# Kernel tuning notes

Hardware: AMD Instinct MI355X
Metric: run time of the kernel (lower is better)

The kernel has to match this reference:

```python
import jax, jax.numpy as jnp
import numpy as np

E, H, M, IN, T = 4, 64, 64, 32, 32      # e_size, hidden_state, message, in_size, target
HL = (128, 256, 128)                     # NNet hidden layers (priba's NNet default)
N_LAYERS = 3


def setup_inputs() -> dict:
    key = jax.random.key(0)
    ks = iter(jax.random.split(key, 64))
    B, N = 16, 128

    def w(shape, scale=0.1):
        return jax.random.normal(next(ks), shape, dtype=jnp.float32) * scale

    inp = {
        "h_in": jax.random.normal(next(ks), (B, N, IN), dtype=jnp.float32),
        "am": jax.random.normal(next(ks), (B, N, N, E), dtype=jnp.float32),
        "g_size": jax.random.randint(next(ks), (B,), 0, N),
    }
    # EdgeNetwork NNet: E -> 128 -> 256 -> 128 -> M*H
    dims_e = (E,) + HL + (M * H,)
    for i in range(4):
        inp[f"We{i}"] = w((dims_e[i], dims_e[i + 1]))
        inp[f"be{i}"] = w((dims_e[i + 1],))
    # GRU (torch nn.GRU, one layer, one step): input M, hidden H
    inp["Wih"] = w((3 * H, M)); inp["Whh"] = w((3 * H, H))
    inp["bih"] = w((3 * H,)); inp["bhh"] = w((3 * H,))
    # Readout NNets: i on [h_T, h_0] (H+IN -> T), j on h_T (H -> T)
    dims_i = (H + IN,) + HL + (T,)
    dims_j = (H,) + HL + (T,)
    for i in range(4):
        inp[f"Wi{i}"] = w((dims_i[i], dims_i[i + 1])); inp[f"bi{i}"] = w((dims_i[i + 1],))
        inp[f"Wj{i}"] = w((dims_j[i], dims_j[i + 1])); inp[f"bj{i}"] = w((dims_j[i + 1],))
    return inp


def _mlp(x, Ws, bs):
    for Wk, bk in zip(Ws[:-1], bs[:-1]):
        x = jax.nn.relu(x @ Wk + bk)
    return x @ Ws[-1] + bs[-1]


def reference(h_in, am, g_size,
              We0, be0, We1, be1, We2, be2, We3, be3,
              Wih, Whh, bih, bhh,
              Wi0, bi0, Wi1, bi1, Wi2, bi2, Wi3, bi3,
              Wj0, bj0, Wj1, bj1, Wj2, bj2, Wj3, bj3):
    B, N, _ = h_in.shape
    h = jnp.pad(h_in, ((0, 0), (0, 0), (0, H - IN)))            # pad to hidden size
    mask = (jnp.arange(N)[None, :] < g_size[:, None]).astype(h.dtype)[:, :, None]  # [B,N,1]

    # Edge-network hidden features; final linear layer is fused into the
    # message contraction to avoid materializing per-edge [M,H] matrices.
    f = am                                                       # [B,N,N,E]
    for Wk, bk in ((We0, be0), (We1, be1), (We2, be2)):
        f = jax.nn.relu(f @ Wk + bk)                             # [B,N,N,128]
    W3 = We3.reshape(HL[-1], M, H)                               # [128,M,H]
    b3 = be3.reshape(M, H)

    for _ in range(N_LAYERS):                                    # weight-tied GGNN steps
        # m[b,v,o] = sum_w (A(e_bvw) @ h_bw)[o], A = reshape(f @ We3 + be3)
        t = jnp.einsum('bvwk,bwi->bvki', f, h)                   # [B,N,128,H]
        msg = jnp.einsum('bvki,koi->bvo', t, W3)
        msg = msg + jnp.einsum('oi,bi->bo', b3, h.sum(1))[:, None, :]
        # single-step torch GRU update
        gi = msg @ Wih.T + bih
        gh = h @ Whh.T + bhh
        r = jax.nn.sigmoid(gi[..., :H] + gh[..., :H])
        z = jax.nn.sigmoid(gi[..., H:2 * H] + gh[..., H:2 * H])
        n = jnp.tanh(gi[..., 2 * H:] + r * gh[..., 2 * H:])
        h = (1.0 - z) * n + z * h
        h = h * mask

    # GGNN readout: sum_v mask * sigmoid(i([h_T, h_0])) * j(h_T), then log_softmax
    gate = jax.nn.sigmoid(_mlp(jnp.concatenate([h, h_in], -1),
                               (Wi0, Wi1, Wi2, Wi3), (bi0, bi1, bi2, bi3)))
    val = _mlp(h, (Wj0, Wj1, Wj2, Wj3), (bj0, bj1, bj2, bj3))
    res = (mask * gate * val).sum(1)                             # [B,T]
    return jax.nn.log_softmax(res, axis=1)
```

## Files before the change

kernel.cpp:

```cpp
#include <hip/hip_runtime.h>
#include <math.h>

#define B   16
#define N   128
#define E   4
#define H   64
#define M   64
#define IN_ 32
#define T   32
#define K1  128
#define K2  256
#define K3  128

typedef _Float16 f16;
typedef f16  f16x8 __attribute__((ext_vector_type(8)));
typedef float f32x4 __attribute__((ext_vector_type(4)));

#define MFMA16(a, b, c) __builtin_amdgcn_mfma_f32_16x16x32_f16(a, b, c, 0, 0, 0)

#define OFF_W1T   0
#define OFF_W2T   32768
#define OFF_WE3H  65536
#define OFF_RI0   589824
#define OFF_RI1   602112
#define OFF_RI2   634880
#define OFF_RI3   667648
#define OFF_RJ0   671744
#define OFF_RJ1   679936
#define OFF_RJ2   712704
#define OFF_RJ3   745472
#define WPACK_SZ  749568

union SmemU {
    struct { float xl[64][4]; f16 y1[64][136]; f16 y2[64][264]; } e;
    struct { f16 Al[128][72]; f16 Bl[128][72]; f16 Ol[128][136]; } pg;
    struct { float prt[4][64]; float hsum[64]; float bias[64]; } bi;
};

__global__ __launch_bounds__(256) void prep_kernel(
    const float* __restrict__ h_in,
    const float* __restrict__ We1, const float* __restrict__ We2,
    const float* __restrict__ We3,
    const float* __restrict__ Wi0, const float* __restrict__ Wi1,
    const float* __restrict__ Wi2, const float* __restrict__ Wi3,
    const float* __restrict__ Wj0, const float* __restrict__ Wj1,
    const float* __restrict__ Wj2, const float* __restrict__ Wj3,
    float* __restrict__ h, f16* __restrict__ h16, f16* __restrict__ hin16,
    f16* __restrict__ wp) {
    int idx = blockIdx.x * 256 + threadIdx.x;
    if (idx < B * N * H) {
        int i  = idx & (H - 1);
        int bn = idx >> 6;
        float v = (i < IN_) ? h_in[bn * IN_ + i] : 0.f;
        h[idx] = v;
        h16[idx] = (f16)v;
        if (i < IN_) hin16[bn * IN_ + i] = (f16)v;
    }
    if (idx >= WPACK_SZ) return;
    if (idx < OFF_W2T) {
        int j = idx >> 7, k = idx & 127;
        wp[idx] = (f16)We1[k * 256 + j];
    } else if (idx < OFF_WE3H) {
        int t = idx - OFF_W2T;
        int j = t >> 8, k = t & 255;
        wp[idx] = (f16)We2[k * 128 + j];
    } else if (idx < OFF_RI0) {
        wp[idx] = (f16)We3[idx - OFF_WE3H];
    } else if (idx < OFF_RI1) {
        int t = idx - OFF_RI0;
        int n = t / 96, c = t % 96;
        wp[idx] = (f16)Wi0[c * 128 + n];
    } else if (idx < OFF_RI2) {
        int t = idx - OFF_RI1;
        int n = t >> 7, k = t & 127;
        wp[idx] = (f16)Wi1[k * 256 + n];
    } else if (idx < OFF_RI3) {
        int t = idx - OFF_RI2;
        int n = t >> 8, k = t & 255;
        wp[idx] = (f16)Wi2[k * 128 + n];
    } else if (idx < OFF_RJ0) {
        int t = idx - OFF_RI3;
        int n = t >> 7, k = t & 127;
        wp[idx] = (f16)Wi3[k * 32 + n];
    } else if (idx < OFF_RJ1) {
        int t = idx - OFF_RJ0;
        int n = t >> 6, c = t & 63;
        wp[idx] = (f16)Wj0[c * 128 + n];
    } else if (idx < OFF_RJ2) {
        int t = idx - OFF_RJ1;
        int n = t >> 7, k = t & 127;
        wp[idx] = (f16)Wj1[k * 256 + n];
    } else if (idx < OFF_RJ3) {
        int t = idx - OFF_RJ2;
        int n = t >> 8, k = t & 255;
        wp[idx] = (f16)Wj2[k * 128 + n];
    } else {
        int t = idx - OFF_RJ3;
        int n = t >> 7, k = t & 127;
        wp[idx] = (f16)Wj3[k * 32 + n];
    }
}


__device__ void edge_body(SmemU& su, int tid, int tile,
                          const float* __restrict__ am,
                          const float* __restrict__ We0,
                          const float* __restrict__ be0,
                          const f16* __restrict__ W1t,
                          const float* __restrict__ be1,
                          const f16* __restrict__ W2t,
                          const float* __restrict__ be2,
                          f16* __restrict__ f) {
    int lane = tid & 63, wv = tid >> 6;
    long long g0 = (long long)tile * 64;

    ((float*)su.e.xl)[tid] = am[g0 * 4 + tid];
    __syncthreads();

    {
        int j = tid & 127, e0 = (tid >> 7) * 32;
        float w0 = We0[j], w1 = We0[128 + j], w2 = We0[256 + j], w3 = We0[384 + j];
        float bb = be0[j];
        #pragma unroll 8
        for (int e = e0; e < e0 + 32; ++e) {
            float v = bb + su.e.xl[e][0] * w0 + su.e.xl[e][1] * w1
                         + su.e.xl[e][2] * w2 + su.e.xl[e][3] * w3;
            su.e.y1[e][j] = (f16)fmaxf(v, 0.f);
        }
    }
    __syncthreads();

    int m = lane & 15, q = lane >> 4;

    {
        f32x4 acc[4][4];
        #pragma unroll
        for (int ct = 0; ct < 4; ++ct)
            #pragma unroll
            for (int rt = 0; rt < 4; ++rt) acc[ct][rt] = (f32x4){0.f, 0.f, 0.f, 0.f};
        #pragma unroll
        for (int s = 0; s < 4; ++s) {
            int k0 = s * 32 + q * 8;
            f16x8 afr[4], bfr[4];
            #pragma unroll
            for (int rt = 0; rt < 4; ++rt)
                afr[rt] = *(const f16x8*)&su.e.y1[rt * 16 + m][k0];
            #pragma unroll
            for (int ct = 0; ct < 4; ++ct) {
                int n = (wv * 4 + ct) * 16 + m;
                bfr[ct] = *(const f16x8*)(W1t + n * 128 + k0);
            }
            #pragma unroll
            for (int ct = 0; ct < 4; ++ct)
                #pragma unroll
                for (int rt = 0; rt < 4; ++rt)
                    acc[ct][rt] = MFMA16(afr[rt], bfr[ct], acc[ct][rt]);
        }
        #pragma unroll
        for (int ct = 0; ct < 4; ++ct) {
            int n = (wv * 4 + ct) * 16 + m;
            float bb = be1[n];
            #pragma unroll
            for (int rt = 0; rt < 4; ++rt)
                #pragma unroll
                for (int r = 0; r < 4; ++r) {
                    int row = rt * 16 + q * 4 + r;
                    su.e.y2[row][n] = (f16)fmaxf(acc[ct][rt][r] + bb, 0.f);
                }
        }
    }
    __syncthreads();

    {
        f32x4 acc[2][4];
        #pragma unroll
        for (int ct = 0; ct < 2; ++ct)
            #pragma unroll
            for (int rt = 0; rt < 4; ++rt) acc[ct][rt] = (f32x4){0.f, 0.f, 0.f, 0.f};
        #pragma unroll
        for (int s = 0; s < 8; ++s) {
            int k0 = s * 32 + q * 8;
            f16x8 afr[4], bfr[2];
            #pragma unroll
            for (int rt = 0; rt < 4; ++rt)
                afr[rt] = *(const f16x8*)&su.e.y2[rt * 16 + m][k0];
            #pragma unroll
            for (int ct = 0; ct < 2; ++ct) {
                int n = (wv * 2 + ct) * 16 + m;
                bfr[ct] = *(const f16x8*)(W2t + n * 256 + k0);
            }
            #pragma unroll
            for (int ct = 0; ct < 2; ++ct)
                #pragma unroll
                for (int rt = 0; rt < 4; ++rt)
                    acc[ct][rt] = MFMA16(afr[rt], bfr[ct], acc[ct][rt]);
        }
        #pragma unroll
        for (int ct = 0; ct < 2; ++ct) {
            int n = (wv * 2 + ct) * 16 + m;
            float bb = be2[n];
            #pragma unroll
            for (int rt = 0; rt < 4; ++rt)
                #pragma unroll
                for (int r = 0; r < 4; ++r) {
                    int row = rt * 16 + q * 4 + r;
                    su.e.y1[row][n] = (f16)fmaxf(acc[ct][rt][r] + bb, 0.f);
                }
        }
    }
    __syncthreads();

    #pragma unroll
    for (int j = 0; j < 4; ++j) {
        int c = tid + j * 256;
        int e = c >> 4, pp = c & 15;
        *(uint4*)(f + (g0 + e) * 128 + pp * 8) = *(const uint4*)&su.e.y1[e][pp * 8];
    }
}

__device__ void pgemm_body(SmemU& su, int tid, int ob, int nt,
                           const f16* __restrict__ h16,
                           const f16* __restrict__ We3h,
                           f16* __restrict__ P2) {
    int lane = tid & 63, wv = tid >> 6;

    #pragma unroll
    for (int j = 0; j < 4; ++j) {
        int c = tid + j * 256;
        int row = c >> 3, pp = c & 7;
        *(uint4*)&su.pg.Al[row][pp * 8] =
            *(const uint4*)(h16 + (size_t)(nt * 128 + row) * 64 + pp * 8);
    }
    #pragma unroll
    for (int j = 0; j < 4; ++j) {
        int c = tid + j * 256;
        int k = c >> 3, pp = c & 7;
        *(uint4*)&su.pg.Bl[k][pp * 8] =
            *(const uint4*)(We3h + ((size_t)(k * 64 + ob)) * 64 + pp * 8);
    }
    __syncthreads();

    int m = lane & 15, q = lane >> 4;
    f32x4 acc[2][8];
    #pragma unroll
    for (int ct = 0; ct < 2; ++ct)
        #pragma unroll
        for (int rt = 0; rt < 8; ++rt) acc[ct][rt] = (f32x4){0.f, 0.f, 0.f, 0.f};
    #pragma unroll
    for (int s = 0; s < 2; ++s) {
        int k0 = s * 32 + q * 8;
        f16x8 afr[8], bfr[2];
        #pragma unroll
        for (int rt = 0; rt < 8; ++rt)
            afr[rt] = *(const f16x8*)&su.pg.Al[rt * 16 + m][k0];
        #pragma unroll
        for (int ct = 0; ct < 2; ++ct)
            bfr[ct] = *(const f16x8*)&su.pg.Bl[(wv * 2 + ct) * 16 + m][k0];
        #pragma unroll
        for (int ct = 0; ct < 2; ++ct)
            #pragma unroll
            for (int rt = 0; rt < 8; ++rt)
                acc[ct][rt] = MFMA16(afr[rt], bfr[ct], acc[ct][rt]);
    }
    #pragma unroll
    for (int ct = 0; ct < 2; ++ct) {
        int col = (wv * 2 + ct) * 16 + m;
        #pragma unroll
        for (int rt = 0; rt < 8; ++rt)
            #pragma unroll
            for (int r = 0; r < 4; ++r)
                su.pg.Ol[rt * 16 + q * 4 + r][col] = (f16)acc[ct][rt][r];
    }
    __syncthreads();
    #pragma unroll
    for (int j = 0; j < 8; ++j) {
        int c = tid + j * 256;
        int row = c >> 4, pp = c & 15;
        *(uint4*)(P2 + ((size_t)(nt * 128 + row) * 64 + ob) * 128 + pp * 8) =
            *(const uint4*)&su.pg.Ol[row][pp * 8];
    }
}

__device__ void bias_body(SmemU& su, int tid, int b,
                          const float* __restrict__ h,
                          const float* __restrict__ be3,
                          float* __restrict__ biasb) {
    int i = tid & 63, wq = tid >> 6;
    float s = 0.f;
    for (int w = wq; w < N; w += 4) s += h[((size_t)(b * N + w)) * H + i];
    su.bi.prt[wq][i] = s;
    __syncthreads();
    if (tid < 64)
        su.bi.hsum[tid] = su.bi.prt[0][tid] + su.bi.prt[1][tid]
                        + su.bi.prt[2][tid] + su.bi.prt[3][tid];
    __syncthreads();
    if (tid < 64) {
        float sb = 0.f;
        #pragma unroll 4
        for (int ii = 0; ii < H; ++ii) sb += be3[tid * H + ii] * su.bi.hsum[ii];
        biasb[b * 64 + tid] = sb;
    }
}

__global__ __launch_bounds__(256, 2) void mega0_kernel(
    const float* __restrict__ am,
    const float* __restrict__ We0, const float* __restrict__ be0,
    const float* __restrict__ be1, const float* __restrict__ be2,
    const float* __restrict__ be3,
    const f16* __restrict__ wp,
    const float* __restrict__ h, const f16* __restrict__ h16,
    f16* __restrict__ f, f16* __restrict__ P2, float* __restrict__ biasb) {
    __shared__ SmemU su;
    int tid = threadIdx.x;
    int bid = blockIdx.x;
    if (bid < 4096) {
        edge_body(su, tid, bid, am, We0, be0, wp + OFF_W1T, be1, wp + OFF_W2T,
                  be2, f);
    } else if (bid < 5120) {
        int t = bid - 4096;
        pgemm_body(su, tid, t & 63, t >> 6, h16, wp + OFF_WE3H, P2);
    } else {
        bias_body(su, tid, bid - 5120, h, be3, biasb);
    }
}

__global__ __launch_bounds__(256, 2) void pg_bias_kernel(
    const float* __restrict__ be3, const f16* __restrict__ wp,
    const float* __restrict__ h, const f16* __restrict__ h16,
    f16* __restrict__ P2, float* __restrict__ biasb) {
    __shared__ SmemU su;
    int tid = threadIdx.x;
    int bid = blockIdx.x;
    if (bid < 1024) {
        pgemm_body(su, tid, bid & 63, bid >> 6, h16, wp + OFF_WE3H, P2);
    } else {
        bias_body(su, tid, bid - 1024, h, be3, biasb);
    }
}

__global__ __launch_bounds__(256, 2) void msg_mfma(
    const f16* __restrict__ f, const f16* __restrict__ P2,
    float* __restrict__ part) {
    __shared__ f16 Al[128][136];
    __shared__ f16 Bl[64][136];
    int tid = threadIdx.x, lane = tid & 63, wv = tid >> 6;
    int ws = blockIdx.x;
    int b  = blockIdx.y;
    int m = lane & 15, q = lane >> 4;

    f32x4 acc[2][4];
    #pragma unroll
    for (int rt = 0; rt < 2; ++rt)
        #pragma unroll
        for (int ct = 0; ct < 4; ++ct) acc[rt][ct] = (f32x4){0.f, 0.f, 0.f, 0.f};

    for (int wi = 0; wi < 4; ++wi) {
        int w = ws * 4 + wi;
        #pragma unroll
        for (int j = 0; j < 8; ++j) {
            int c = tid + j * 256;
            int v = c >> 4, pp = c & 15;
            *(uint4*)&Al[v][pp * 8] =
                *(const uint4*)(f + (((size_t)(b * 128 + v) * 128 + w) * 128) + pp * 8);
        }
        #pragma unroll
        for (int j = 0; j < 4; ++j) {
            int c = tid + j * 256;
            int o = c >> 4, pp = c & 15;
            *(uint4*)&Bl[o][pp * 8] =
                *(const uint4*)(P2 + (((size_t)(b * 128 + w) * 64 + o) * 128) + pp * 8);
        }
        __syncthreads();
        #pragma unroll
        for (int s = 0; s < 4; ++s) {
            int k0 = s * 32 + q * 8;
            f16x8 afr[2], bfr[4];
            #pragma unroll
            for (int rt = 0; rt < 2; ++rt)
                afr[rt] = *(const f16x8*)&Al[(wv * 2 + rt) * 16 + m][k0];
            #pragma unroll
            for (int ct = 0; ct < 4; ++ct)
                bfr[ct] = *(const f16x8*)&Bl[ct * 16 + m][k0];
            #pragma unroll
            for (int rt = 0; rt < 2; ++rt)
                #pragma unroll
                for (int ct = 0; ct < 4; ++ct)
                    acc[rt][ct] = MFMA16(afr[rt], bfr[ct], acc[rt][ct]);
        }
        __syncthreads();
    }
    float* pp = part + (size_t)ws * (2048 * 64);
    #pragma unroll
    for (int rt = 0; rt < 2; ++rt)
        #pragma unroll
        for (int ct = 0; ct < 4; ++ct) {
            int o = ct * 16 + m;
            #pragma unroll
            for (int r = 0; r < 4; ++r) {
                int v = (wv * 2 + rt) * 16 + q * 4 + r;
                pp[(size_t)(b * 128 + v) * 64 + o] = acc[rt][ct][r];
            }
        }
}

__global__ __launch_bounds__(192) void gru_kernel(
    const float* __restrict__ biasb, const float* __restrict__ part,
    float* __restrict__ h, f16* __restrict__ h16,
    const float* __restrict__ Wih, const float* __restrict__ Whh,
    const float* __restrict__ bih, const float* __restrict__ bhh,
    const int* __restrict__ g_size) {
    __shared__ float m_lds[M];
    __shared__ float h_lds[H];
    __shared__ float gi[3 * H], gh[3 * H];
    int tid = threadIdx.x;
    int bv  = blockIdx.x;
    int b = bv >> 7, v = bv & 127;

    if (tid < M) {
        float s = biasb[b * 64 + tid];
        #pragma unroll 8
        for (int sp = 0; sp < 32; ++sp)
            s += part[(size_t)sp * (2048 * 64) + bv * 64 + tid];
        m_lds[tid] = s;
    } else if (tid < M + H) {
        h_lds[tid - M] = h[bv * H + (tid - M)];
    }
    __syncthreads();

    {
        float si = bih[tid], sh = bhh[tid];
        const float* wi = Wih + tid * M;
        const float* wh = Whh + tid * H;
        #pragma unroll 4
        for (int k = 0; k < M; ++k) si += wi[k] * m_lds[k];
        #pragma unroll 4
        for (int k = 0; k < H; ++k) sh += wh[k] * h_lds[k];
        gi[tid] = si;
        gh[tid] = sh;
    }
    __syncthreads();
    if (tid < H) {
        float r = 1.f / (1.f + expf(-(gi[tid] + gh[tid])));
        float z = 1.f / (1.f + expf(-(gi[H + tid] + gh[H + tid])));
        float n = tanhf(gi[2 * H + tid] + r * gh[2 * H + tid]);
        float hv = (1.f - z) * n + z * h_lds[tid];
        float maskf = (v < g_size[b]) ? 1.f : 0.f;
        hv *= maskf;
        h[bv * H + tid] = hv;
        h16[bv * H + tid] = (f16)hv;
    }
}

__global__ __launch_bounds__(256, 4) void readout_mfma(
    const f16* __restrict__ h16, const f16* __restrict__ hin16,
    const int* __restrict__ g_size, const f16* __restrict__ wp,
    const float* __restrict__ bi0, const float* __restrict__ bi1,
    const float* __restrict__ bi2, const float* __restrict__ bi3,
    const float* __restrict__ bj0, const float* __restrict__ bj1,
    const float* __restrict__ bj2, const float* __restrict__ bj3,
    float* __restrict__ contrib) {
    __shared__ f16 Xl[32][104];
    __shared__ f16 A1[32][136];
    __shared__ f16 A2[32][264];
    __shared__ float Gl[32][36];
    const f16* Ri0 = wp + OFF_RI0; const f16* Ri1 = wp + OFF_RI1;
    const f16* Ri2 = wp + OFF_RI2; const f16* Ri3 = wp + OFF_RI3;
    const f16* Rj0 = wp + OFF_RJ0; const f16* Rj1 = wp + OFF_RJ1;
    const f16* Rj2 = wp + OFF_RJ2; const f16* Rj3 = wp + OFF_RJ3;
    int tid = threadIdx.x, lane = tid & 63, wv = tid >> 6;
    int m = lane & 15, q = lane >> 4;
    int r0 = blockIdx.x * 32;

    {
        int row = tid >> 3, pp = tid & 7;
        *(uint4*)&Xl[row][pp * 8] = *(const uint4*)(h16 + (size_t)(r0 + row) * 64 + pp * 8);
        if (tid < 128) {
            int row2 = tid >> 2, p2 = tid & 3;
            *(uint4*)&Xl[row2][64 + p2 * 8] =
                *(const uint4*)(hin16 + (size_t)(r0 + row2) * 32 + p2 * 8);
        }
    }
    __syncthreads();

    {
        f32x4 acc[2][2];
        #pragma unroll
        for (int ct = 0; ct < 2; ++ct)
            #pragma unroll
            for (int rt = 0; rt < 2; ++rt) acc[ct][rt] = (f32x4){0.f, 0.f, 0.f, 0.f};
        #pragma unroll
        for (int s = 0; s < 3; ++s) {
            int k0 = s * 32 + q * 8;
            f16x8 afr[2], bfr[2];
            #pragma unroll
            for (int rt = 0; rt < 2; ++rt) afr[rt] = *(const f16x8*)&Xl[rt * 16 + m][k0];
            #pragma unroll
            for (int ct = 0; ct < 2; ++ct)
                bfr[ct] = *(const f16x8*)(Ri0 + ((wv * 2 + ct) * 16 + m) * 96 + k0);
            #pragma unroll
            for (int ct = 0; ct < 2; ++ct)
                #pragma unroll
                for (int rt = 0; rt < 2; ++rt)
                    acc[ct][rt] = MFMA16(afr[rt], bfr[ct], acc[ct][rt]);
        }
        #pragma unroll
        for (int ct = 0; ct < 2; ++ct) {
            int n = (wv * 2 + ct) * 16 + m;
            float bb = bi0[n];
            #pragma unroll
            for (int rt = 0; rt < 2; ++rt)
                #pragma unroll
                for (int r = 0; r < 4; ++r)
                    A1[rt * 16 + q * 4 + r][n] = (f16)fmaxf(acc[ct][rt][r] + bb, 0.f);
        }
    }
    __syncthreads();

    {
        f32x4 acc[4][2];
        #pragma unroll
        for (int ct = 0; ct < 4; ++ct)
            #pragma unroll
            for (int rt = 0; rt < 2; ++rt) acc[ct][rt] = (f32x4){0.f, 0.f, 0.f, 0.f};
        #pragma unroll
        for (int s = 0; s < 4; ++s) {
            int k0 = s * 32 + q * 8;
            f16x8 afr[2], bfr[4];
            #pragma unroll
            for (int rt = 0; rt < 2; ++rt) afr[rt] = *(const f16x8*)&A1[rt * 16 + m][k0];
            #pragma unroll
            for (int ct = 0; ct < 4; ++ct)
                bfr[ct] = *(const f16x8*)(Ri1 + ((wv * 4 + ct) * 16 + m) * 128 + k0);
            #pragma unroll
            for (int ct = 0; ct < 4; ++ct)
                #pragma unroll
                for (int rt = 0; rt < 2; ++rt)
                    acc[ct][rt] = MFMA16(afr[rt], bfr[ct], acc[ct][rt]);
        }
        #pragma unroll
        for (int ct = 0; ct < 4; ++ct) {
            int n = (wv * 4 + ct) * 16 + m;
            float bb = bi1[n];
            #pragma unroll
            for (int rt = 0; rt < 2; ++rt)
                #pragma unroll
                for (int r = 0; r < 4; ++r)
                    A2[rt * 16 + q * 4 + r][n] = (f16)fmaxf(acc[ct][rt][r] + bb, 0.f);
        }
    }
    __syncthreads();

    {
        f32x4 acc[2][2];
        #pragma unroll
        for (int ct = 0; ct < 2; ++ct)
            #pragma unroll
            for (int rt = 0; rt < 2; ++rt) acc[ct][rt] = (f32x4){0.f, 0.f, 0.f, 0.f};
        #pragma unroll
        for (int s = 0; s < 8; ++s) {
            int k0 = s * 32 + q * 8;
            f16x8 afr[2], bfr[2];
            #pragma unroll
            for (int rt = 0; rt < 2; ++rt) afr[rt] = *(const f16x8*)&A2[rt * 16 + m][k0];
            #pragma unroll
            for (int ct = 0; ct < 2; ++ct)
                bfr[ct] = *(const f16x8*)(Ri2 + ((wv * 2 + ct) * 16 + m) * 256 + k0);
            #pragma unroll
            for (int ct = 0; ct < 2; ++ct)
                #pragma unroll
                for (int rt = 0; rt < 2; ++rt)
                    acc[ct][rt] = MFMA16(afr[rt], bfr[ct], acc[ct][rt]);
        }
        __syncthreads();
        #pragma unroll
        for (int ct = 0; ct < 2; ++ct) {
            int n = (wv * 2 + ct) * 16 + m;
            float bb = bi2[n];
            #pragma unroll
            for (int rt = 0; rt < 2; ++rt)
                #pragma unroll
                for (int r = 0; r < 4; ++r)
                    A1[rt * 16 + q * 4 + r][n] = (f16)fmaxf(acc[ct][rt][r] + bb, 0.f);
        }
    }
    __syncthreads();

    if (wv < 2) {
        f32x4 acc[2];
        acc[0] = (f32x4){0.f, 0.f, 0.f, 0.f};
        acc[1] = (f32x4){0.f, 0.f, 0.f, 0.f};
        int n = wv * 16 + m;
        #pragma unroll
        for (int s = 0; s < 4; ++s) {
            int k0 = s * 32 + q * 8;
            f16x8 bfr = *(const f16x8*)(Ri3 + n * 128 + k0);
            #pragma unroll
            for (int rt = 0; rt < 2; ++rt) {
                f16x8 afr = *(const f16x8*)&A1[rt * 16 + m][k0];
                acc[rt] = MFMA16(afr, bfr, acc[rt]);
            }
        }
        float bb = bi3[n];
        #pragma unroll
        for (int rt = 0; rt < 2; ++rt)
            #pragma unroll
            for (int r = 0; r < 4; ++r)
                Gl[rt * 16 + q * 4 + r][n] = 1.f / (1.f + expf(-(acc[rt][r] + bb)));
    }
    __syncthreads();

    {
        f32x4 acc[2][2];
        #pragma unroll
        for (int ct = 0; ct < 2; ++ct)
            #pragma unroll
            for (int rt = 0; rt < 2; ++rt) acc[ct][rt] = (f32x4){0.f, 0.f, 0.f, 0.f};
        #pragma unroll
        for (int s = 0; s < 2; ++s) {
            int k0 = s * 32 + q * 8;
            f16x8 afr[2], bfr[2];
            #pragma unroll
            for (int rt = 0; rt < 2; ++rt) afr[rt] = *(const f16x8*)&Xl[rt * 16 + m][k0];
            #pragma unroll
            for (int ct = 0; ct < 2; ++ct)
                bfr[ct] = *(const f16x8*)(Rj0 + ((wv * 2 + ct) * 16 + m) * 64 + k0);
            #pragma unroll
            for (int ct = 0; ct < 2; ++ct)
                #pragma unroll
                for (int rt = 0; rt < 2; ++rt)
                    acc[ct][rt] = MFMA16(afr[rt], bfr[ct], acc[ct][rt]);
        }
        __syncthreads();
        #pragma unroll
        for (int ct = 0; ct < 2; ++ct) {
            int n = (wv * 2 + ct) * 16 + m;
            float bb = bj0[n];
            #pragma unroll
            for (int rt = 0; rt < 2; ++rt)
                #pragma unroll
                for (int r = 0; r < 4; ++r)
                    A1[rt * 16 + q * 4 + r][n] = (f16)fmaxf(acc[ct][rt][r] + bb, 0.f);
        }
    }
    __syncthreads();

    {
        f32x4 acc[4][2];
        #pragma unroll
        for (int ct = 0; ct < 4; ++ct)
            #pragma unroll
            for (int rt = 0; rt < 2; ++rt) acc[ct][rt] = (f32x4){0.f, 0.f, 0.f, 0.f};
        #pragma unroll
        for (int s = 0; s < 4; ++s) {
            int k0 = s * 32 + q * 8;
            f16x8 afr[2], bfr[4];
            #pragma unroll
            for (int rt = 0; rt < 2; ++rt) afr[rt] = *(const f16x8*)&A1[rt * 16 + m][k0];
            #pragma unroll
            for (int ct = 0; ct < 4; ++ct)
                bfr[ct] = *(const f16x8*)(Rj1 + ((wv * 4 + ct) * 16 + m) * 128 + k0);
            #pragma unroll
            for (int ct = 0; ct < 4; ++ct)
                #pragma unroll
                for (int rt = 0; rt < 2; ++rt)
                    acc[ct][rt] = MFMA16(afr[rt], bfr[ct], acc[ct][rt]);
        }
        #pragma unroll
        for (int ct = 0; ct < 4; ++ct) {
            int n = (wv * 4 + ct) * 16 + m;
            float bb = bj1[n];
            #pragma unroll
            for (int rt = 0; rt < 2; ++rt)
                #pragma unroll
                for (int r = 0; r < 4; ++r)
                    A2[rt * 16 + q * 4 + r][n] = (f16)fmaxf(acc[ct][rt][r] + bb, 0.f);
        }
    }
    __syncthreads();

    {
        f32x4 acc[2][2];
        #pragma unroll
        for (int ct = 0; ct < 2; ++ct)
            #pragma unroll
            for (int rt = 0; rt < 2; ++rt) acc[ct][rt] = (f32x4){0.f, 0.f, 0.f, 0.f};
        #pragma unroll
        for (int s = 0; s < 8; ++s) {
            int k0 = s * 32 + q * 8;
            f16x8 afr[2], bfr[2];
            #pragma unroll
            for (int rt = 0; rt < 2; ++rt) afr[rt] = *(const f16x8*)&A2[rt * 16 + m][k0];
            #pragma unroll
            for (int ct = 0; ct < 2; ++ct)
                bfr[ct] = *(const f16x8*)(Rj2 + ((wv * 2 + ct) * 16 + m) * 256 + k0);
            #pragma unroll
            for (int ct = 0; ct < 2; ++ct)
                #pragma unroll
                for (int rt = 0; rt < 2; ++rt)
                    acc[ct][rt] = MFMA16(afr[rt], bfr[ct], acc[ct][rt]);
        }
        __syncthreads();
        #pragma unroll
        for (int ct = 0; ct < 2; ++ct) {
            int n = (wv * 2 + ct) * 16 + m;
            float bb = bj2[n];
            #pragma unroll
            for (int rt = 0; rt < 2; ++rt)
                #pragma unroll
                for (int r = 0; r < 4; ++r)
                    A1[rt * 16 + q * 4 + r][n] = (f16)fmaxf(acc[ct][rt][r] + bb, 0.f);
        }
    }
    __syncthreads();

    if (wv < 2) {
        f32x4 acc[2];
        acc[0] = (f32x4){0.f, 0.f, 0.f, 0.f};
        acc[1] = (f32x4){0.f, 0.f, 0.f, 0.f};
        int n = wv * 16 + m;
        #pragma unroll
        for (int s = 0; s < 4; ++s) {
            int k0 = s * 32 + q * 8;
            f16x8 bfr = *(const f16x8*)(Rj3 + n * 128 + k0);
            #pragma unroll
            for (int rt = 0; rt < 2; ++rt) {
                f16x8 afr = *(const f16x8*)&A1[rt * 16 + m][k0];
                acc[rt] = MFMA16(afr, bfr, acc[rt]);
            }
        }
        float bb = bj3[n];
        #pragma unroll
        for (int rt = 0; rt < 2; ++rt)
            #pragma unroll
            for (int r = 0; r < 4; ++r) {
                int row = rt * 16 + q * 4 + r;
                int rg = r0 + row;
                int b = rg >> 7, v = rg & 127;
                float maskf = (v < g_size[b]) ? 1.f : 0.f;
                contrib[(size_t)rg * T + n] = maskf * Gl[row][n] * (acc[rt][r] + bb);
            }
    }
}

__global__ __launch_bounds__(64) void finalize_kernel(const float* __restrict__ contrib,
                                                      float* __restrict__ out) {
    __shared__ float res[T];
    int b = blockIdx.x;
    int o = threadIdx.x;
    if (o < T) {
        float s = 0.f;
        for (int v = 0; v < N; ++v) s += contrib[(b * N + v) * T + o];
        res[o] = s;
    }
    __syncthreads();
    if (o < T) {
        float mx = res[0];
        for (int i = 1; i < T; ++i) mx = fmaxf(mx, res[i]);
        float se = 0.f;
        for (int i = 0; i < T; ++i) se += expf(res[i] - mx);
        out[b * T + o] = res[o] - mx - logf(se);
    }
}

extern "C" void kernel_launch(void* const* d_in, const int* in_sizes, int n_in,
                              void* d_out, int out_size, void* d_ws, size_t ws_size,
                              hipStream_t stream) {
    (void)in_sizes; (void)n_in; (void)out_size; (void)ws_size;
    const float* h_in = (const float*)d_in[0];
    const float* am   = (const float*)d_in[1];
    const int*   g_sz = (const int*)d_in[2];
    const float* We0 = (const float*)d_in[3],  *be0 = (const float*)d_in[4];
    const float* We1 = (const float*)d_in[5],  *be1 = (const float*)d_in[6];
    const float* We2 = (const float*)d_in[7],  *be2 = (const float*)d_in[8];
    const float* We3 = (const float*)d_in[9],  *be3 = (const float*)d_in[10];
    const float* Wih = (const float*)d_in[11], *Whh = (const float*)d_in[12];
    const float* bih = (const float*)d_in[13], *bhh = (const float*)d_in[14];
    const float* Wi0 = (const float*)d_in[15], *bi0 = (const float*)d_in[16];
    const float* Wj0 = (const float*)d_in[17], *bj0 = (const float*)d_in[18];
    const float* Wi1 = (const float*)d_in[19], *bi1 = (const float*)d_in[20];
    const float* Wj1 = (const float*)d_in[21], *bj1 = (const float*)d_in[22];
    const float* Wi2 = (const float*)d_in[23], *bi2 = (const float*)d_in[24];
    const float* Wj2 = (const float*)d_in[25], *bj2 = (const float*)d_in[26];
    const float* Wi3 = (const float*)d_in[27], *bi3 = (const float*)d_in[28];
    const float* Wj3 = (const float*)d_in[29], *bj3 = (const float*)d_in[30];

    float* out = (float*)d_out;

    f16*   f    = (f16*)d_ws;
    f16*   P2   = f + (size_t)33554432;
    float* part = (float*)(P2 + (size_t)16777216);
    float* h    = part + (size_t)4194304;
    float* biasb = h + 131072;
    float* contrib = biasb + 1024;
    f16*   h16  = (f16*)(contrib + 65536);
    f16*   hin16 = h16 + 131072;
    f16*   wp   = hin16 + 65536;

    prep_kernel<<<(WPACK_SZ + 255) / 256, 256, 0, stream>>>(
        h_in, We1, We2, We3, Wi0, Wi1, Wi2, Wi3, Wj0, Wj1, Wj2, Wj3,
        h, h16, hin16, wp);

    mega0_kernel<<<4096 + 1024 + 16, 256, 0, stream>>>(
        am, We0, be0, be1, be2, be3, wp, h, h16, f, P2, biasb);
    msg_mfma<<<dim3(32, 16), 256, 0, stream>>>(f, P2, part);
    gru_kernel<<<B * N, 192, 0, stream>>>(biasb, part, h, h16,
                                          Wih, Whh, bih, bhh, g_sz);

    for (int l = 1; l < 3; ++l) {
        pg_bias_kernel<<<1024 + 16, 256, 0, stream>>>(be3, wp, h, h16, P2, biasb);
        msg_mfma<<<dim3(32, 16), 256, 0, stream>>>(f, P2, part);
        gru_kernel<<<B * N, 192, 0, stream>>>(biasb, part, h, h16,
                                              Wih, Whh, bih, bhh, g_sz);
    }

    readout_mfma<<<64, 256, 0, stream>>>(h16, hin16, g_sz, wp,
                                         bi0, bi1, bi2, bi3,
                                         bj0, bj1, bj2, bj3, contrib);
    finalize_kernel<<<B, 64, 0, stream>>>(contrib, out);
}
```

Baseline: 412.1 us.

## Fuse message GEMM with GRU update and fold finalize into readout

Replaces the split-K message kernel plus separate GRU kernel with one kernel per (batch, 32-node tile). It accumulates messages over all neighbours in registers and then applies the GRU in place, which removes the fp32 partial-sum buffer and its reduction. The P-GEMM tile is halved to 64 rows to double its block count, and occupancy hints are raised. The log-softmax finalize moves into the last readout block via an atomic counter. The fused message kernel launches only 64 blocks that loop serially over 128 neighbours with two barriers each, so it risks leaving most of the GPU idle.

```diff
diff --git a/kernel.cpp b/kernel.cpp
--- a/kernel.cpp
+++ b/kernel.cpp
@@ -8,9 +8,6 @@
 #define M   64
 #define IN_ 32
 #define T   32
-#define K1  128
-#define K2  256
-#define K3  128
 
 typedef _Float16 f16;
 typedef f16  f16x8 __attribute__((ext_vector_type(8)));
@@ -33,8 +30,8 @@
 
 union SmemU {
     struct { float xl[64][4]; f16 y1[64][136]; f16 y2[64][264]; } e;
-    struct { f16 Al[128][72]; f16 Bl[128][72]; f16 Ol[128][136]; } pg;
-    struct { float prt[4][64]; float hsum[64]; float bias[64]; } bi;
+    struct { f16 Al[64][72]; f16 Bl[128][72]; f16 Ol[64][136]; } pg;
+    struct { float prt[4][64]; float hsum[64]; } bi;
 };
 
 __global__ __launch_bounds__(256) void prep_kernel(
@@ -225,11 +222,11 @@
     int lane = tid & 63, wv = tid >> 6;
 
     #pragma unroll
-    for (int j = 0; j < 4; ++j) {
+    for (int j = 0; j < 2; ++j) {
         int c = tid + j * 256;
         int row = c >> 3, pp = c & 7;
         *(uint4*)&su.pg.Al[row][pp * 8] =
-            *(const uint4*)(h16 + (size_t)(nt * 128 + row) * 64 + pp * 8);
+            *(const uint4*)(h16 + (size_t)(nt * 64 + row) * 64 + pp * 8);
     }
     #pragma unroll
     for (int j = 0; j < 4; ++j) {
@@ -241,17 +238,17 @@
     __syncthreads();
 
     int m = lane & 15, q = lane >> 4;
-    f32x4 acc[2][8];
+    f32x4 acc[2][4];
     #pragma unroll
     for (int ct = 0; ct < 2; ++ct)
         #pragma unroll
-        for (int rt = 0; rt < 8; ++rt) acc[ct][rt] = (f32x4){0.f, 0.f, 0.f, 0.f};
+        for (int rt = 0; rt < 4; ++rt) acc[ct][rt] = (f32x4){0.f, 0.f, 0.f, 0.f};
     #pragma unroll
     for (int s = 0; s < 2; ++s) {
         int k0 = s * 32 + q * 8;
-        f16x8 afr[8], bfr[2];
-        #pragma unroll
-        for (int rt = 0; rt < 8; ++rt)
+        f16x8 afr[4], bfr[2];
+        #pragma unroll
+        for (int rt = 0; rt < 4; ++rt)
             afr[rt] = *(const f16x8*)&su.pg.Al[rt * 16 + m][k0];
         #pragma unroll
         for (int ct = 0; ct < 2; ++ct)
@@ -259,24 +256,24 @@
         #pragma unroll
         for (int ct = 0; ct < 2; ++ct)
             #pragma unroll
-            for (int rt = 0; rt < 8; ++rt)
+            for (int rt = 0; rt < 4; ++rt)
                 acc[ct][rt] = MFMA16(afr[rt], bfr[ct], acc[ct][rt]);
     }
     #pragma unroll
     for (int ct = 0; ct < 2; ++ct) {
         int col = (wv * 2 + ct) * 16 + m;
         #pragma unroll
-        for (int rt = 0; rt < 8; ++rt)
+        for (int rt = 0; rt < 4; ++rt)
             #pragma unroll
             for (int r = 0; r < 4; ++r)
                 su.pg.Ol[rt * 16 + q * 4 + r][col] = (f16)acc[ct][rt][r];
     }
     __syncthreads();
     #pragma unroll
-    for (int j = 0; j < 8; ++j) {
+    for (int j = 0; j < 4; ++j) {
         int c = tid + j * 256;
         int row = c >> 4, pp = c & 15;
-        *(uint4*)(P2 + ((size_t)(nt * 128 + row) * 64 + ob) * 128 + pp * 8) =
+        *(uint4*)(P2 + ((size_t)(nt * 64 + row) * 64 + ob) * 128 + pp * 8) =
             *(const uint4*)&su.pg.Ol[row][pp * 8];
     }
 }
@@ -302,7 +299,7 @@
     }
 }
 
-__global__ __launch_bounds__(256, 2) void mega0_kernel(
+__global__ __launch_bounds__(256, 3) void mega0_kernel(
     const float* __restrict__ am,
     const float* __restrict__ We0, const float* __restrict__ be0,
     const float* __restrict__ be1, const float* __restrict__ be2,
@@ -316,153 +313,141 @@
     if (bid < 4096) {
         edge_body(su, tid, bid, am, We0, be0, wp + OFF_W1T, be1, wp + OFF_W2T,
                   be2, f);
-    } else if (bid < 5120) {
+    } else if (bid < 6144) {
         int t = bid - 4096;
         pgemm_body(su, tid, t & 63, t >> 6, h16, wp + OFF_WE3H, P2);
     } else {
-        bias_body(su, tid, bid - 5120, h, be3, biasb);
+        bias_body(su, tid, bid - 6144, h, be3, biasb);
     }
 }
 
-__global__ __launch_bounds__(256, 2) void pg_bias_kernel(
+__global__ __launch_bounds__(256, 3) void pg_bias_kernel(
     const float* __restrict__ be3, const f16* __restrict__ wp,
     const float* __restrict__ h, const f16* __restrict__ h16,
     f16* __restrict__ P2, float* __restrict__ biasb) {
     __shared__ SmemU su;
     int tid = threadIdx.x;
     int bid = blockIdx.x;
-    if (bid < 1024) {
+    if (bid < 2048) {
         pgemm_body(su, tid, bid & 63, bid >> 6, h16, wp + OFF_WE3H, P2);
     } else {
-        bias_body(su, tid, bid - 1024, h, be3, biasb);
+        bias_body(su, tid, bid - 2048, h, be3, biasb);
     }
 }
 
-__global__ __launch_bounds__(256, 2) void msg_mfma(
+__global__ __launch_bounds__(256, 2) void msggru_kernel(
     const f16* __restrict__ f, const f16* __restrict__ P2,
-    float* __restrict__ part) {
-    __shared__ f16 Al[128][136];
-    __shared__ f16 Bl[64][136];
-    int tid = threadIdx.x, lane = tid & 63, wv = tid >> 6;
-    int ws = blockIdx.x;
-    int b  = blockIdx.y;
-    int m = lane & 15, q = lane >> 4;
-
-    f32x4 acc[2][4];
-    #pragma unroll
-    for (int rt = 0; rt < 2; ++rt)
-        #pragma unroll
-        for (int ct = 0; ct < 4; ++ct) acc[rt][ct] = (f32x4){0.f, 0.f, 0.f, 0.f};
-
-    for (int wi = 0; wi < 4; ++wi) {
-        int w = ws * 4 + wi;
-        #pragma unroll
-        for (int j = 0; j < 8; ++j) {
-            int c = tid + j * 256;
-            int v = c >> 4, pp = c & 15;
-            *(uint4*)&Al[v][pp * 8] =
-                *(const uint4*)(f + (((size_t)(b * 128 + v) * 128 + w) * 128) + pp * 8);
-        }
-        #pragma unroll
-        for (int j = 0; j < 4; ++j) {
-            int c = tid + j * 256;
-            int o = c >> 4, pp = c & 15;
-            *(uint4*)&Bl[o][pp * 8] =
-                *(const uint4*)(P2 + (((size_t)(b * 128 + w) * 64 + o) * 128) + pp * 8);
-        }
-        __syncthreads();
-        #pragma unroll
-        for (int s = 0; s < 4; ++s) {
-            int k0 = s * 32 + q * 8;
-            f16x8 afr[2], bfr[4];
-            #pragma unroll
-            for (int rt = 0; rt < 2; ++rt)
-                afr[rt] = *(const f16x8*)&Al[(wv * 2 + rt) * 16 + m][k0];
-            #pragma unroll
-            for (int ct = 0; ct < 4; ++ct)
-                bfr[ct] = *(const f16x8*)&Bl[ct * 16 + m][k0];
-            #pragma unroll
-            for (int rt = 0; rt < 2; ++rt)
-                #pragma unroll
-                for (int ct = 0; ct < 4; ++ct)
-                    acc[rt][ct] = MFMA16(afr[rt], bfr[ct], acc[rt][ct]);
-        }
-        __syncthreads();
-    }
-    float* pp = part + (size_t)ws * (2048 * 64);
-    #pragma unroll
-    for (int rt = 0; rt < 2; ++rt)
-        #pragma unroll
-        for (int ct = 0; ct < 4; ++ct) {
-            int o = ct * 16 + m;
-            #pragma unroll
-            for (int r = 0; r < 4; ++r) {
-                int v = (wv * 2 + rt) * 16 + q * 4 + r;
-                pp[(size_t)(b * 128 + v) * 64 + o] = acc[rt][ct][r];
-            }
-        }
-}
-
-__global__ __launch_bounds__(192) void gru_kernel(
-    const float* __restrict__ biasb, const float* __restrict__ part,
+    const float* __restrict__ biasb,
     float* __restrict__ h, f16* __restrict__ h16,
     const float* __restrict__ Wih, const float* __restrict__ Whh,
     const float* __restrict__ bih, const float* __restrict__ bhh,
     const int* __restrict__ g_size) {
-    __shared__ float m_lds[M];
-    __shared__ float h_lds[H];
-    __shared__ float gi[3 * H], gh[3 * H];
-    int tid = threadIdx.x;
-    int bv  = blockIdx.x;
-    int b = bv >> 7, v = bv & 127;
-
-    if (tid < M) {
-        float s = biasb[b * 64 + tid];
-        #pragma unroll 8
-        for (int sp = 0; sp < 32; ++sp)
-            s += part[(size_t)sp * (2048 * 64) + bv * 64 + tid];
-        m_lds[tid] = s;
-    } else if (tid < M + H) {
-        h_lds[tid - M] = h[bv * H + (tid - M)];
-    }
-    __syncthreads();
-
-    {
-        float si = bih[tid], sh = bhh[tid];
-        const float* wi = Wih + tid * M;
-        const float* wh = Whh + tid * H;
+    __shared__ union {
+        struct { f16 Al[32][136]; f16 Bl[64][136]; } st;
+        struct { float msg[32][68]; float hl[32][64]; } gr;
+    } su;
+    int tid = threadIdx.x, lane = tid & 63, wv = tid >> 6;
+    int m = lane & 15, q = lane >> 4;
+    int vt = blockIdx.x;
+    int b  = blockIdx.y;
+    int v0 = vt * 32;
+
+    f32x4 acc[2];
+    acc[0] = (f32x4){0.f, 0.f, 0.f, 0.f};
+    acc[1] = (f32x4){0.f, 0.f, 0.f, 0.f};
+
+    for (int w = 0; w < N; ++w) {
+        #pragma unroll
+        for (int j = 0; j < 2; ++j) {
+            int c = tid + j * 256;
+            int v = c >> 4, pp = c & 15;
+            *(uint4*)&su.st.Al[v][pp * 8] =
+                *(const uint4*)(f + (((size_t)(b * 128 + v0 + v) * 128 + w) * 128) + pp * 8);
+        }
+        #pragma unroll
+        for (int j = 0; j < 4; ++j) {
+            int c = tid + j * 256;
+            int o = c >> 4, pp = c & 15;
+            *(uint4*)&su.st.Bl[o][pp * 8] =
+                *(const uint4*)(P2 + (((size_t)(b * 128 + w) * 64 + o) * 128) + pp * 8);
+        }
+        __syncthreads();
+        #pragma unroll
+        for (int s = 0; s < 4; ++s) {
+            int k0 = s * 32 + q * 8;
+            f16x8 bfr = *(const f16x8*)&su.st.Bl[wv * 16 + m][k0];
+            #pragma unroll
+            for (int rt = 0; rt < 2; ++rt) {
+                f16x8 afr = *(const f16x8*)&su.st.Al[rt * 16 + m][k0];
+                acc[rt] = MFMA16(afr, bfr, acc[rt]);
+            }
+        }
+        __syncthreads();
+    }
+
+    #pragma unroll
+    for (int rt = 0; rt < 2; ++rt)
+        #pragma unroll
+        for (int r = 0; r < 4; ++r) {
+            int row = rt * 16 + q * 4 + r;
+            int o = wv * 16 + m;
+            su.gr.msg[row][o] = acc[rt][r] + biasb[b * 64 + o];
+        }
+    #pragma unroll
+    for (int j = 0; j < 8; ++j) {
+        int c = tid + j * 256;
+        int n = c >> 6, i = c & 63;
+        su.gr.hl[n][i] = h[((size_t)(b * 128 + v0 + n)) * 64 + i];
+    }
+    __syncthreads();
+
+    int gs = g_size[b];
+    #pragma unroll
+    for (int j = 0; j < 8; ++j) {
+        int c = tid + j * 256;
+        int n = c >> 6, i = c & 63;
+        float sr = bih[i], sz = bih[64 + i], sn = bih[128 + i];
+        float tr = bhh[i], tz = bhh[64 + i], tn = bhh[128 + i];
+        const float* wr = Wih + i * 64;
+        const float* wz = Wih + (64 + i) * 64;
+        const float* wn = Wih + (128 + i) * 64;
+        const float* ur = Whh + i * 64;
+        const float* uz = Whh + (64 + i) * 64;
+        const float* un = Whh + (128 + i) * 64;
         #pragma unroll 4
-        for (int k = 0; k < M; ++k) si += wi[k] * m_lds[k];
-        #pragma unroll 4
-        for (int k = 0; k < H; ++k) sh += wh[k] * h_lds[k];
-        gi[tid] = si;
-        gh[tid] = sh;
-    }
-    __syncthreads();
-    if (tid < H) {
-        float r = 1.f / (1.f + expf(-(gi[tid] + gh[tid])));
-        float z = 1.f / (1.f + expf(-(gi[H + tid] + gh[H + tid])));
-        float n = tanhf(gi[2 * H + tid] + r * gh[2 * H + tid]);
-        float hv = (1.f - z) * n + z * h_lds[tid];
-        float maskf = (v < g_size[b]) ? 1.f : 0.f;
+        for (int k = 0; k < 64; ++k) {
+            float mk = su.gr.msg[n][k];
+            float hk = su.gr.hl[n][k];
+            sr += wr[k] * mk;  sz += wz[k] * mk;  sn += wn[k] * mk;
+            tr += ur[k] * hk;  tz += uz[k] * hk;  tn += un[k] * hk;
+        }
+        float r = 1.f / (1.f + expf(-(sr + tr)));
+        float z = 1.f / (1.f + expf(-(sz + tz)));
+        float nn = tanhf(sn + r * tn);
+        float hv = (1.f - z) * nn + z * su.gr.hl[n][i];
+        float maskf = ((v0 + n) < gs) ? 1.f : 0.f;
         hv *= maskf;
-        h[bv * H + tid] = hv;
-        h16[bv * H + tid] = (f16)hv;
+        size_t row = (size_t)(b * 128 + v0 + n);
+        h[row * 64 + i] = hv;
+        h16[row * 64 + i] = (f16)hv;
     }
 }
 
-__global__ __launch_bounds__(256, 4) void readout_mfma(
+__global__ __launch_bounds__(256, 4) void readout_final(
     const f16* __restrict__ h16, const f16* __restrict__ hin16,
     const int* __restrict__ g_size, const f16* __restrict__ wp,
     const float* __restrict__ bi0, const float* __restrict__ bi1,
     const float* __restrict__ bi2, const float* __restrict__ bi3,
     const float* __restrict__ bj0, const float* __restrict__ bj1,
     const float* __restrict__ bj2, const float* __restrict__ bj3,
-    float* __restrict__ contrib) {
+    float* __restrict__ contrib, float* __restrict__ out,
+    int* __restrict__ done) {
     __shared__ f16 Xl[32][104];
     __shared__ f16 A1[32][136];
     __shared__ f16 A2[32][264];
     __shared__ float Gl[32][36];
+    __shared__ float fin[T];
+    __shared__ int lastflag;
     const f16* Ri0 = wp + OFF_RI0; const f16* Ri1 = wp + OFF_RI1;
     const f16* Ri2 = wp + OFF_RI2; const f16* Ri3 = wp + OFF_RI3;
     const f16* Rj0 = wp + OFF_RJ0; const f16* Rj1 = wp + OFF_RJ1;
@@ -735,30 +720,33 @@
             for (int r = 0; r < 4; ++r) {
                 int row = rt * 16 + q * 4 + r;
                 int rg = r0 + row;
-                int b = rg >> 7, v = rg & 127;
-                float maskf = (v < g_size[b]) ? 1.f : 0.f;
+                int bb2 = rg >> 7, v = rg & 127;
+                float maskf = (v < g_size[bb2]) ? 1.f : 0.f;
                 contrib[(size_t)rg * T + n] = maskf * Gl[row][n] * (acc[rt][r] + bb);
             }
     }
-}
-
-__global__ __launch_bounds__(64) void finalize_kernel(const float* __restrict__ contrib,
-                                                      float* __restrict__ out) {
-    __shared__ float res[T];
-    int b = blockIdx.x;
-    int o = threadIdx.x;
-    if (o < T) {
-        float s = 0.f;
-        for (int v = 0; v < N; ++v) s += contrib[(b * N + v) * T + o];
-        res[o] = s;
-    }
-    __syncthreads();
-    if (o < T) {
-        float mx = res[0];
-        for (int i = 1; i < T; ++i) mx = fmaxf(mx, res[i]);
-        float se = 0.f;
-        for (int i = 0; i < T; ++i) se += expf(res[i] - mx);
-        out[b * T + o] = res[o] - mx - logf(se);
+
+    __syncthreads();
+    __threadfence();
+    if (tid == 0) lastflag = (atomicAdd(done, 1) == 63);
+    __syncthreads();
+    if (!lastflag) return;
+    __threadfence();
+    for (int b = 0; b < B; ++b) {
+        if (tid < T) {
+            float s = 0.f;
+            for (int v = 0; v < N; ++v) s += contrib[(b * N + v) * T + tid];
+            fin[tid] = s;
+        }
+        __syncthreads();
+        if (tid < T) {
+            float mx = fin[0];
+            for (int i = 1; i < T; ++i) mx = fmaxf(mx, fin[i]);
+            float se = 0.f;
+            for (int i = 0; i < T; ++i) se += expf(fin[i] - mx);
+            out[b * T + tid] = fin[tid] - mx - logf(se);
+        }
+        __syncthreads();
     }
 }
 
@@ -786,35 +774,33 @@
 
     float* out = (float*)d_out;
 
-    f16*   f    = (f16*)d_ws;
+    int*   done = (int*)d_ws;
+    f16*   f    = (f16*)((char*)d_ws + 1024);
     f16*   P2   = f + (size_t)33554432;
-    float* part = (float*)(P2 + (size_t)16777216);
-    float* h    = part + (size_t)4194304;
+    float* h    = (float*)(P2 + (size_t)16777216);
     float* biasb = h + 131072;
     float* contrib = biasb + 1024;
     f16*   h16  = (f16*)(contrib + 65536);
     f16*   hin16 = h16 + 131072;
     f16*   wp   = hin16 + 65536;
 
+    hipMemsetAsync(d_ws, 0, 1024, stream);
     prep_kernel<<<(WPACK_SZ + 255) / 256, 256, 0, stream>>>(
         h_in, We1, We2, We3, Wi0, Wi1, Wi2, Wi3, Wj0, Wj1, Wj2, Wj3,
         h, h16, hin16, wp);
 
-    mega0_kernel<<<4096 + 1024 + 16, 256, 0, stream>>>(
+    mega0_kernel<<<4096 + 2048 + 16, 256, 0, stream>>>(
         am, We0, be0, be1, be2, be3, wp, h, h16, f, P2, biasb);
-    msg_mfma<<<dim3(32, 16), 256, 0, stream>>>(f, P2, part);
-    gru_kernel<<<B * N, 192, 0, stream>>>(biasb, part, h, h16,
-                                          Wih, Whh, bih, bhh, g_sz);
+    msggru_kernel<<<dim3(4, 16), 256, 0, stream>>>(f, P2, biasb, h, h16,
+                                                   Wih, Whh, bih, bhh, g_sz);
 
     for (int l = 1; l < 3; ++l) {
-        pg_bias_kernel<<<1024 + 16, 256, 0, stream>>>(be3, wp, h, h16, P2, biasb);
-        msg_mfma<<<dim3(32, 16), 256, 0, stream>>>(f, P2, part);
-        gru_kernel<<<B * N, 192, 0, stream>>>(biasb, part, h, h16,
-                                              Wih, Whh, bih, bhh, g_sz);
-    }
-
-    readout_mfma<<<64, 256, 0, stream>>>(h16, hin16, g_sz, wp,
-                                         bi0, bi1, bi2, bi3,
-                                         bj0, bj1, bj2, bj3, contrib);
-    finalize_kernel<<<B, 64, 0, stream>>>(contrib, out);
+        pg_bias_kernel<<<2048 + 16, 256, 0, stream>>>(be3, wp, h, h16, P2, biasb);
+        msggru_kernel<<<dim3(4, 16), 256, 0, stream>>>(f, P2, biasb, h, h16,
+                                                       Wih, Whh, bih, bhh, g_sz);
+    }
+
+    readout_final<<<64, 256, 0, stream>>>(h16, hin16, g_sz, wp,
+                                          bi0, bi1, bi2, bi3,
+                                          bj0, bj1, bj2, bj3, contrib, out, done);
 }
```

Measured after the change: 1.095 ms. +165.6%, slower.
